# Performance work log

Hardware: AMD Instinct MI355X
Metric: run time of the kernel (lower is better)

Reference implementation:

```python
import jax, jax.numpy as jnp
import numpy as np

N_NODES = 100000
N_EDGES = 1600000
N_FEAT = 16
HEADS = 4


def _feast_conv(x, src, dst, U, c, W, b):
    """FeaStConv: q = softmax_h(u^T(x_j - x_i) + c); out_i = mean_j sum_h q_h * (W_h x_j) + b."""
    n = x.shape[0]
    e = src.shape[0]
    xj = x[src]                                   # [E, Fin] gather
    q = jax.nn.softmax(jnp.matmul(xj - x[dst], U) + c, axis=-1)   # [E, H]
    xs = jnp.matmul(xj, W).reshape(e, HEADS, -1)  # [E, H, Fout]
    msg = jnp.einsum('eh,eho->eo', q, xs)         # [E, Fout]
    deg = jax.ops.segment_sum(jnp.ones((e,), x.dtype), dst, num_segments=n)
    agg = jax.ops.segment_sum(msg, dst, num_segments=n)
    return agg / jnp.maximum(deg, 1.0)[:, None] + b


def setup_inputs() -> dict:
    key = jax.random.key(0)
    ks = jax.random.split(key, 32)
    s = 0.1
    d = {
        'x': jax.random.normal(ks[0], (N_NODES, N_FEAT), jnp.float32),
        'edge_index': jax.random.randint(ks[1], (2, N_EDGES), 0, N_NODES, jnp.int32),
        # conv1: 16 -> 16
        'U1': jax.random.normal(ks[2], (N_FEAT, HEADS), jnp.float32) * s,
        'c1': jnp.zeros((HEADS,), jnp.float32),
        'W1': jax.random.normal(ks[3], (N_FEAT, HEADS * 16), jnp.float32) * s,
        'b1': jnp.zeros((16,), jnp.float32),
        # conv2: 16 -> 32
        'U2': jax.random.normal(ks[4], (16, HEADS), jnp.float32) * s,
        'c2': jnp.zeros((HEADS,), jnp.float32),
        'W2': jax.random.normal(ks[5], (16, HEADS * 32), jnp.float32) * s,
        'b2': jnp.zeros((32,), jnp.float32),
        # conv3: 32 -> 64
        'U3': jax.random.normal(ks[6], (32, HEADS), jnp.float32) * s,
        'c3': jnp.zeros((HEADS,), jnp.float32),
        'W3': jax.random.normal(ks[7], (32, HEADS * 64), jnp.float32) * s,
        'b3': jnp.zeros((64,), jnp.float32),
        # linear tail 64->32->16->8->4->1
        'lw1': jax.random.normal(ks[8], (64, 32), jnp.float32) * s,
        'lb1': jnp.zeros((32,), jnp.float32),
        'lw2': jax.random.normal(ks[9], (32, 16), jnp.float32) * s,
        'lb2': jnp.zeros((16,), jnp.float32),
        'lw3': jax.random.normal(ks[10], (16, 8), jnp.float32) * s,
        'lb3': jnp.zeros((8,), jnp.float32),
        'lw4': jax.random.normal(ks[11], (8, 4), jnp.float32) * s,
        'lb4': jnp.zeros((4,), jnp.float32),
        'lw5': jax.random.normal(ks[12], (4, 1), jnp.float32) * s,
        'lb5': jnp.zeros((1,), jnp.float32),
    }
    return d


def reference(x, edge_index, U1, c1, W1, b1, U2, c2, W2, b2, U3, c3, W3, b3,
              lw1, lb1, lw2, lb2, lw3, lb3, lw4, lb4, lw5, lb5):
    src, dst = edge_index[0], edge_index[1]
    h = jax.nn.relu(_feast_conv(x, src, dst, U1, c1, W1, b1))
    h = jax.nn.relu(_feast_conv(h, src, dst, U2, c2, W2, b2))
    h = jax.nn.relu(_feast_conv(h, src, dst, U3, c3, W3, b3))
    # dropout disabled (inference / drop_bool=False): Linear+ReLU tail
    h = jax.nn.relu(jnp.matmul(h, lw1) + lb1)
    h = jax.nn.relu(jnp.matmul(h, lw2) + lb2)
    h = jax.nn.relu(jnp.matmul(h, lw3) + lb3)
    h = jax.nn.relu(jnp.matmul(h, lw4) + lb4)
    return jax.nn.sigmoid(jnp.matmul(h, lw5) + lb5)   # [N, 1]
```

## Files before the change

### kernel.cpp

```cpp
#include <hip/hip_runtime.h>
#include <math.h>

#define N_NODES 100000
#define N_EDGES 1600000
#define HEADS 4
#define NBKT ((N_NODES + 255) / 256)
#define CHUNK_E 4096
#define NCHUNK ((N_EDGES + CHUNK_E - 1) / CHUNK_E)
#define GN ((N_NODES + 255) / 256)

typedef unsigned short ushort_t;
typedef unsigned char  uchar_t;

__device__ __forceinline__ ushort_t f2bf(float x) {
    unsigned u = __float_as_uint(x);
    u += 0x7FFF + ((u >> 16) & 1);
    return (ushort_t)(u >> 16);
}
__device__ __forceinline__ float bf2f(ushort_t v) {
    return __uint_as_float(((unsigned)v) << 16);
}
__device__ __forceinline__ void unpack2(unsigned u, float& lo, float& hi) {
    lo = __uint_as_float(u << 16);
    hi = __uint_as_float(u & 0xffff0000u);
}
__device__ __forceinline__ uchar_t f2fp8(float x) {
    if (x <= 0.0f) return 0;
    unsigned u = __float_as_uint(x) + (1u << 19);
    int e = (int)(u >> 23) - 127 + 15;
    if (e <= 0) return 0;
    if (e > 31) return (uchar_t)255;
    return (uchar_t)((e << 3) | ((u >> 20) & 7));
}
__device__ __forceinline__ float fp8d(uchar_t b) {
    unsigned v = (((unsigned)(b >> 3) + 112u) << 23) | ((unsigned)(b & 7) << 20);
    return (b == 0) ? 0.0f : __uint_as_float(v);
}


__global__ __launch_bounds__(256) void bhist_pcast_kernel(
        const int* __restrict__ dst, int* __restrict__ hist_rows,
        const float* __restrict__ x, const float* __restrict__ U,
        float* __restrict__ p, ushort_t* __restrict__ xbf)
{
    __shared__ int h[NBKT];
    if (blockIdx.x < NCHUNK) {
        for (int i = threadIdx.x; i < NBKT; i += 256) h[i] = 0;
        __syncthreads();
        int base = blockIdx.x * CHUNK_E;
        #pragma unroll
        for (int j = 0; j < CHUNK_E / 256; j++) {
            int e = base + j * 256 + threadIdx.x;
            if (e < N_EDGES) atomicAdd(&h[dst[e] >> 8], 1);
        }
        __syncthreads();
        for (int i = threadIdx.x; i < NBKT; i += 256)
            hist_rows[(size_t)blockIdx.x * NBKT + i] = h[i];
    } else {
        int n = (blockIdx.x - NCHUNK) * 256 + threadIdx.x;
        if (n >= N_NODES) return;
        float a0 = 0, a1 = 0, a2 = 0, a3 = 0;
        const float* hr = x + (size_t)n * 16;
        float xv[16];
        #pragma unroll
        for (int f = 0; f < 16; f++) {
            xv[f] = hr[f];
            a0 += xv[f] * U[f * 4 + 0];
            a1 += xv[f] * U[f * 4 + 1];
            a2 += xv[f] * U[f * 4 + 2];
            a3 += xv[f] * U[f * 4 + 3];
        }
        *(float4*)(p + (size_t)n * 4) = make_float4(a0, a1, a2, a3);
        #pragma unroll
        for (int j = 0; j < 4; j++) {
            ushort4 u;
            u.x = f2bf(xv[4 * j + 0]); u.y = f2bf(xv[4 * j + 1]);
            u.z = f2bf(xv[4 * j + 2]); u.w = f2bf(xv[4 * j + 3]);
            *(ushort4*)(xbf + (size_t)n * 16 + 4 * j) = u;
        }
    }
}


__global__ __launch_bounds__(512) void bscan_kernel(const int* __restrict__ hist_rows,
                                                    int* __restrict__ bucket_base,
                                                    int* __restrict__ bucket_cursor) {
    __shared__ int tmp[512];
    int i = threadIdx.x;
    int v = 0;
    if (i < NBKT)
        for (int r = 0; r < NCHUNK; r++) v += hist_rows[(size_t)r * NBKT + i];
    tmp[i] = v;
    __syncthreads();
    for (int off = 1; off < 512; off <<= 1) {
        int t = (i >= off) ? tmp[i - off] : 0;
        __syncthreads();
        tmp[i] += t;
        __syncthreads();
    }
    int excl = tmp[i] - v;
    if (i < NBKT) { bucket_base[i] = excl; bucket_cursor[i] = excl; }
    if (i == NBKT) bucket_base[NBKT] = N_EDGES;
}


__global__ __launch_bounds__(256) void partition_kernel(const int* __restrict__ src,
                                                        const int* __restrict__ dst,
                                                        int* __restrict__ bucket_cursor,
                                                        int* __restrict__ csr_tmp) {
    constexpr int EPT = CHUNK_E / 256;
    __shared__ int h[NBKT];
    __shared__ int gbase[NBKT];
    __shared__ int rcnt[NBKT];
    for (int i = threadIdx.x; i < NBKT; i += 256) { h[i] = 0; rcnt[i] = 0; }
    __syncthreads();
    int base = blockIdx.x * CHUNK_E;
    int d[EPT], s[EPT];
    #pragma unroll
    for (int j = 0; j < EPT; j++) {
        int e = base + j * 256 + threadIdx.x;
        d[j] = (e < N_EDGES) ? dst[e] : -1;
        s[j] = (e < N_EDGES) ? src[e] : 0;
        if (d[j] >= 0) atomicAdd(&h[d[j] >> 8], 1);
    }
    __syncthreads();
    for (int i = threadIdx.x; i < NBKT; i += 256)
        if (h[i]) gbase[i] = atomicAdd(&bucket_cursor[i], h[i]);
    __syncthreads();
    #pragma unroll
    for (int j = 0; j < EPT; j++) {
        if (d[j] >= 0) {
            int b = d[j] >> 8;
            int r = atomicAdd(&rcnt[b], 1);
            csr_tmp[gbase[b] + r] = ((d[j] & 255) << 20) | s[j];
        }
    }
}


__global__ __launch_bounds__(256) void bucket_build_kernel(const int* __restrict__ bucket_base,
                                                           const int* __restrict__ csr_tmp,
                                                           int* __restrict__ rowptr,
                                                           int* __restrict__ csr_src) {
    __shared__ int cnt[256];
    __shared__ int tscan[256];
    __shared__ int exc[256];
    __shared__ int stage[8192];
    int b = blockIdx.x;
    int rbeg = bucket_base[b], rend = bucket_base[b + 1];
    int sz = rend - rbeg;
    int tid = threadIdx.x;

    cnt[tid] = 0;
    __syncthreads();
    for (int k = rbeg + tid; k < rend; k += 256) atomicAdd(&cnt[csr_tmp[k] >> 20], 1);
    __syncthreads();
    int v = cnt[tid];
    tscan[tid] = v;
    __syncthreads();
    for (int off = 1; off < 256; off <<= 1) {
        int t = (tid >= off) ? tscan[tid - off] : 0;
        __syncthreads();
        tscan[tid] += t;
        __syncthreads();
    }
    int ex = tscan[tid] - v;
    int node = b * 256 + tid;
    if (node < N_NODES) rowptr[node] = rbeg + ex;
    if (b == 0 && tid == 0) rowptr[N_NODES] = N_EDGES;
    exc[tid] = ex;
    cnt[tid] = 0;
    __syncthreads();

    if (sz <= 8192) {
        for (int k = rbeg + tid; k < rend; k += 256) {
            int pk = csr_tmp[k];
            int dl = pk >> 20;
            int r  = atomicAdd(&cnt[dl], 1);
            stage[exc[dl] + r] = pk & ((1 << 20) - 1);
        }
        __syncthreads();
        for (int i = tid; i < sz; i += 256) csr_src[rbeg + i] = stage[i];
    } else {
        for (int k = rbeg + tid; k < rend; k += 256) {
            int pk = csr_tmp[k];
            int dl = pk >> 20;
            int r  = atomicAdd(&cnt[dl], 1);
            csr_src[rbeg + exc[dl] + r] = pk & ((1 << 20) - 1);
        }
    }
}


template<int FIN, int FMT>
__global__ __launch_bounds__(256) void zgather_kernel(
        const int* __restrict__ rowptr, const int* __restrict__ csr_src,
        const float* __restrict__ p, const float* __restrict__ cvec,
        const void* __restrict__ hraw,
        ushort_t* __restrict__ z)
{
    constexpr int NPB   = 256 / FIN;
    constexpr int CHUNK = 512;
    __shared__ int    sbeg[NPB + 1];
    __shared__ float4 qs[CHUNK];
    __shared__ int    ssrc[CHUNK];

    const ushort_t* hbf = (const ushort_t*)hraw;
    const uchar_t*  hf8 = (const uchar_t*)hraw;

    int tid  = threadIdx.x;
    int nloc = tid / FIN;
    int f    = tid - nloc * FIN;
    int n0   = blockIdx.x * NPB;
    int n    = n0 + nloc;

    if (tid <= NPB) {
        int idx = n0 + tid;
        sbeg[tid] = rowptr[idx > N_NODES ? N_NODES : idx];
    }
    float c0 = cvec[0], c1 = cvec[1], c2 = cvec[2], c3 = cvec[3];
    __syncthreads();

    int BB = sbeg[0], BE = sbeg[NPB];
    int beg = sbeg[nloc], end = sbeg[nloc + 1];
    float a0 = 0, a1 = 0, a2 = 0, a3 = 0;

    for (int cbase = BB; cbase < BE; cbase += CHUNK) {
        int cend = min(cbase + CHUNK, BE);
        __syncthreads();
        for (int k = cbase + tid; k < cend; k += 256) {
            int s = csr_src[k];
            int lo = 0, hi = NPB;
            while (hi - lo > 1) { int mid = (lo + hi) >> 1; if (k < sbeg[mid]) hi = mid; else lo = mid; }
            float4 ps = *(const float4*)(p + (size_t)s * 4);
            float4 pd = *(const float4*)(p + (size_t)(n0 + lo) * 4);
            float l0 = ps.x - pd.x + c0;
            float l1 = ps.y - pd.y + c1;
            float l2 = ps.z - pd.z + c2;
            float l3 = ps.w - pd.w + c3;
            float m  = fmaxf(fmaxf(l0, l1), fmaxf(l2, l3));
            float e0 = __expf(l0 - m), e1 = __expf(l1 - m);
            float e2 = __expf(l2 - m), e3 = __expf(l3 - m);
            float deg = (float)(sbeg[lo + 1] - sbeg[lo]);
            float inv = 1.0f / (fmaxf(deg, 1.0f) * (e0 + e1 + e2 + e3));
            qs[k - cbase]   = make_float4(e0 * inv, e1 * inv, e2 * inv, e3 * inv);
            ssrc[k - cbase] = s;
        }
        __syncthreads();
        int kb = (beg > cbase ? beg : cbase) - cbase;
        int ke = (end < cend ? end : cend) - cbase;
        int k = kb;
        for (; k + 8 <= ke; k += 8) {
            float xv8[8];
            if (FMT == 0) {
                ushort_t u[8];
                #pragma unroll
                for (int j = 0; j < 8; j++) u[j] = hbf[(size_t)ssrc[k + j] * FIN + f];
                #pragma unroll
                for (int j = 0; j < 8; j++) xv8[j] = bf2f(u[j]);
            } else {
                uchar_t u[8];
                #pragma unroll
                for (int j = 0; j < 8; j++) u[j] = hf8[(size_t)ssrc[k + j] * FIN + f];
                #pragma unroll
                for (int j = 0; j < 8; j++) xv8[j] = fp8d(u[j]);
            }
            #pragma unroll
            for (int j = 0; j < 8; j++) {
                float4 q = qs[k + j];
                a0 += q.x * xv8[j]; a1 += q.y * xv8[j];
                a2 += q.z * xv8[j]; a3 += q.w * xv8[j];
            }
        }
        for (; k < ke; k++) {
            float xv = (FMT == 0) ? bf2f(hbf[(size_t)ssrc[k] * FIN + f])
                                  : fp8d(hf8[(size_t)ssrc[k] * FIN + f]);
            float4 q = qs[k];
            a0 += q.x * xv; a1 += q.y * xv; a2 += q.z * xv; a3 += q.w * xv;
        }
    }

    if (n < N_NODES) {
        size_t base = (size_t)n * (4 * FIN) + f;
        z[base]           = f2bf(a0);
        z[base + FIN]     = f2bf(a1);
        z[base + 2 * FIN] = f2bf(a2);
        z[base + 3 * FIN] = f2bf(a3);
    }
}


template<int FIN, int FOUT, int MODE>
__global__ __launch_bounds__(256, 4) void post_kernel(
        const ushort_t* __restrict__ z,
        const float* __restrict__ W,
        const float* __restrict__ b,
        ushort_t* __restrict__ out_bf,
        uchar_t* __restrict__ out_f8,
        const float* __restrict__ Unext,
        float* __restrict__ pnext)
{
    constexpr int K   = 4 * FIN;
    constexpr int OL  = FOUT / 4;
    constexpr int NPB = 4 * (256 / OL);
    constexpr int WSZ = FIN * 4 * FOUT;
    constexpr bool PNEXT = (MODE != 0);
    __shared__ float Wp[WSZ];
    __shared__ float htile[PNEXT ? NPB * FOUT : 1];
    __shared__ float Uloc[PNEXT ? FOUT * 4 : 1];
    for (int i = threadIdx.x; i < WSZ; i += 256) {
        int f = i / (4 * FOUT);
        int r = i - f * (4 * FOUT);
        int h = r / FOUT;
        int o = r - h * FOUT;
        Wp[(h * FIN + f) * FOUT + o] = W[i];
    }
    if (PNEXT) {
        for (int i = threadIdx.x; i < FOUT * 4; i += 256) Uloc[i] = Unext[i];
    }
    __syncthreads();

    int ol = threadIdx.x % OL;
    int g  = threadIdx.x / OL;
    int n0 = blockIdx.x * NPB + g * 4;

    float4 bv = *(const float4*)(b + 4 * ol);
    float4 acc[4];
    const ushort_t* zr[4];
    #pragma unroll
    for (int j = 0; j < 4; j++) {
        acc[j] = make_float4(0.f, 0.f, 0.f, 0.f);
        int nn = n0 + j; if (nn > N_NODES - 1) nn = N_NODES - 1;
        zr[j] = z + (size_t)nn * K;
    }

    #pragma unroll 2
    for (int kq = 0; kq < K / 4; kq++) {
        float zv[4][4];
        #pragma unroll
        for (int j = 0; j < 4; j++) {
            ushort4 zu = *(const ushort4*)(zr[j] + 4 * kq);
            zv[j][0] = bf2f(zu.x); zv[j][1] = bf2f(zu.y);
            zv[j][2] = bf2f(zu.z); zv[j][3] = bf2f(zu.w);
        }
        #pragma unroll
        for (int jj = 0; jj < 4; jj++) {
            float4 wv = *(const float4*)(Wp + (4 * kq + jj) * FOUT + 4 * ol);
            #pragma unroll
            for (int j = 0; j < 4; j++) {
                float s = zv[j][jj];
                acc[j].x += s * wv.x;
                acc[j].y += s * wv.y;
                acc[j].z += s * wv.z;
                acc[j].w += s * wv.w;
            }
        }
    }

    #pragma unroll
    for (int j = 0; j < 4; j++) {
        int nn = n0 + j;
        float4 r;
        r.x = fmaxf(acc[j].x + bv.x, 0.0f);
        r.y = fmaxf(acc[j].y + bv.y, 0.0f);
        r.z = fmaxf(acc[j].z + bv.z, 0.0f);
        r.w = fmaxf(acc[j].w + bv.w, 0.0f);
        if (PNEXT)
            *(float4*)(htile + (g * 4 + j) * FOUT + 4 * ol) = r;
        if (nn < N_NODES) {
            if (MODE == 2) {
                uchar_t u0 = f2fp8(r.x), u1 = f2fp8(r.y), u2 = f2fp8(r.z), u3 = f2fp8(r.w);
                unsigned pk = (unsigned)u0 | ((unsigned)u1 << 8) |
                              ((unsigned)u2 << 16) | ((unsigned)u3 << 24);
                *(unsigned*)(out_f8 + (size_t)nn * FOUT + 4 * ol) = pk;
            } else {
                ushort4 u;
                u.x = f2bf(r.x); u.y = f2bf(r.y); u.z = f2bf(r.z); u.w = f2bf(r.w);
                *(ushort4*)(out_bf + (size_t)nn * FOUT + 4 * ol) = u;
            }
        }
    }

    if (PNEXT) {
        __syncthreads();
        int tid = threadIdx.x;
        if (tid < NPB) {
            int nn = blockIdx.x * NPB + tid;
            if (nn < N_NODES) {
                float a0 = 0, a1 = 0, a2 = 0, a3 = 0;
                const float* hr = htile + tid * FOUT;
                #pragma unroll
                for (int f = 0; f < FOUT; f++) {
                    float xv = hr[f];
                    a0 += xv * Uloc[f * 4 + 0];
                    a1 += xv * Uloc[f * 4 + 1];
                    a2 += xv * Uloc[f * 4 + 2];
                    a3 += xv * Uloc[f * 4 + 3];
                }
                *(float4*)(pnext + (size_t)nn * 4) = make_float4(a0, a1, a2, a3);
            }
        }
    }
}


__global__ __launch_bounds__(256) void tail_kernel(
        const ushort_t* __restrict__ h,
        const float* __restrict__ lw1, const float* __restrict__ lb1,
        const float* __restrict__ lw2, const float* __restrict__ lb2,
        const float* __restrict__ lw3, const float* __restrict__ lb3,
        const float* __restrict__ lw4, const float* __restrict__ lb4,
        const float* __restrict__ lw5, const float* __restrict__ lb5,
        float* __restrict__ out)
{
    __shared__ float w1[64 * 32], w2[32 * 16], w3[16 * 8], w4[8 * 4], w5[4];
    __shared__ float B1[32], B2[16], B3[8], B4[4], B5[1];
    for (int i = threadIdx.x; i < 64 * 32; i += blockDim.x) w1[i] = lw1[i];
    for (int i = threadIdx.x; i < 32 * 16; i += blockDim.x) w2[i] = lw2[i];
    for (int i = threadIdx.x; i < 16 * 8;  i += blockDim.x) w3[i] = lw3[i];
    for (int i = threadIdx.x; i < 8 * 4;   i += blockDim.x) w4[i] = lw4[i];
    for (int i = threadIdx.x; i < 4;       i += blockDim.x) w5[i] = lw5[i];
    for (int i = threadIdx.x; i < 32; i += blockDim.x) B1[i] = lb1[i];
    for (int i = threadIdx.x; i < 16; i += blockDim.x) B2[i] = lb2[i];
    for (int i = threadIdx.x; i < 8;  i += blockDim.x) B3[i] = lb3[i];
    for (int i = threadIdx.x; i < 4;  i += blockDim.x) B4[i] = lb4[i];
    if (threadIdx.x == 0) B5[0] = lb5[0];
    __syncthreads();

    int n = blockIdx.x * blockDim.x + threadIdx.x;
    if (n >= N_NODES) return;

    float a[64];
    const uint4* hrow = (const uint4*)(h + (size_t)n * 64);
    #pragma unroll
    for (int j = 0; j < 8; j++) {
        uint4 v = hrow[j];
        unpack2(v.x, a[8 * j + 0], a[8 * j + 1]);
        unpack2(v.y, a[8 * j + 2], a[8 * j + 3]);
        unpack2(v.z, a[8 * j + 4], a[8 * j + 5]);
        unpack2(v.w, a[8 * j + 6], a[8 * j + 7]);
    }

    float t1[32];
    for (int o = 0; o < 32; o++) {
        float acc = B1[o];
        #pragma unroll
        for (int i = 0; i < 64; i++) acc += a[i] * w1[i * 32 + o];
        t1[o] = fmaxf(acc, 0.0f);
    }
    float t2[16];
    for (int o = 0; o < 16; o++) {
        float acc = B2[o];
        #pragma unroll
        for (int i = 0; i < 32; i++) acc += t1[i] * w2[i * 16 + o];
        t2[o] = fmaxf(acc, 0.0f);
    }
    float t3[8];
    for (int o = 0; o < 8; o++) {
        float acc = B3[o];
        #pragma unroll
        for (int i = 0; i < 16; i++) acc += t2[i] * w3[i * 8 + o];
        t3[o] = fmaxf(acc, 0.0f);
    }
    float t4[4];
    for (int o = 0; o < 4; o++) {
        float acc = B4[o];
        #pragma unroll
        for (int i = 0; i < 8; i++) acc += t3[i] * w4[i * 4 + o];
        t4[o] = fmaxf(acc, 0.0f);
    }
    float zf = B5[0];
    #pragma unroll
    for (int i = 0; i < 4; i++) zf += t4[i] * w5[i];
    out[n] = 1.0f / (1.0f + expf(-zf));
}


extern "C" void kernel_launch(void* const* d_in, const int* in_sizes, int n_in,
                              void* d_out, int out_size, void* d_ws, size_t ws_size,
                              hipStream_t stream) {
    const float* x   = (const float*)d_in[0];
    const int*   ei  = (const int*)d_in[1];
    const int*   src = ei;
    const int*   dst = ei + N_EDGES;
    const float* U1 = (const float*)d_in[2];  const float* c1 = (const float*)d_in[3];
    const float* W1 = (const float*)d_in[4];  const float* b1 = (const float*)d_in[5];
    const float* U2 = (const float*)d_in[6];  const float* c2 = (const float*)d_in[7];
    const float* W2 = (const float*)d_in[8];  const float* b2 = (const float*)d_in[9];
    const float* U3 = (const float*)d_in[10]; const float* c3 = (const float*)d_in[11];
    const float* W3 = (const float*)d_in[12]; const float* b3 = (const float*)d_in[13];
    const float* lw1 = (const float*)d_in[14]; const float* lb1 = (const float*)d_in[15];
    const float* lw2 = (const float*)d_in[16]; const float* lb2 = (const float*)d_in[17];
    const float* lw3 = (const float*)d_in[18]; const float* lb3 = (const float*)d_in[19];
    const float* lw4 = (const float*)d_in[20]; const float* lb4 = (const float*)d_in[21];
    const float* lw5 = (const float*)d_in[22]; const float* lb5 = (const float*)d_in[23];

    char* ws = (char*)d_ws;
    size_t off = 0;
    auto alloc = [&](size_t bytes) -> void* {
        void* ptr = (void*)(ws + off);
        off += (bytes + 255) & ~(size_t)255;
        return ptr;
    };
    int*      hist_rows     = (int*)alloc((size_t)NCHUNK * NBKT * 4);
    int*      bucket_base   = (int*)alloc((size_t)(NBKT + 1) * 4);
    int*      bucket_cursor = (int*)alloc((size_t)NBKT * 4);
    int*      csr_tmp       = (int*)alloc((size_t)N_EDGES * 4);
    int*      rowptr        = (int*)alloc(((size_t)N_NODES + 1) * 4);
    int*      csr_src       = (int*)alloc((size_t)N_EDGES * 4);
    float*    p             = (float*)alloc((size_t)N_NODES * 4 * 4);
    ushort_t* z             = (ushort_t*)alloc((size_t)N_NODES * 128 * 2);
    ushort_t* xbf           = (ushort_t*)alloc((size_t)N_NODES * 16 * 2);
    ushort_t* h1bf          = (ushort_t*)alloc((size_t)N_NODES * 16 * 2);
    uchar_t*  h2f8          = (uchar_t*)alloc((size_t)N_NODES * 32);
    ushort_t* h3bf          = (ushort_t*)alloc((size_t)N_NODES * 64 * 2);
    (void)ws_size;

    const int B = 256;

    bhist_pcast_kernel<<<NCHUNK + GN, B, 0, stream>>>(dst, hist_rows, x, U1, p, xbf);
    bscan_kernel<<<1, 512, 0, stream>>>(hist_rows, bucket_base, bucket_cursor);
    partition_kernel<<<NCHUNK, B, 0, stream>>>(src, dst, bucket_cursor, csr_tmp);
    bucket_build_kernel<<<NBKT, B, 0, stream>>>(bucket_base, csr_tmp, rowptr, csr_src);

    const int ZG16 = (N_NODES + (256 / 16) - 1) / (256 / 16);
    const int ZG32 = (N_NODES + (256 / 32) - 1) / (256 / 32);
    const int NPB1 = 4 * (256 / (16 / 4));
    const int NPB2 = 4 * (256 / (32 / 4));
    const int NPB3 = 4 * (256 / (64 / 4));

    zgather_kernel<16, 0><<<ZG16, B, 0, stream>>>(rowptr, csr_src, p, c1, xbf, z);
    post_kernel<16, 16, 1><<<(N_NODES + NPB1 - 1) / NPB1, B, 0, stream>>>(
        z, W1, b1, h1bf, nullptr, U2, p);

    zgather_kernel<16, 0><<<ZG16, B, 0, stream>>>(rowptr, csr_src, p, c2, h1bf, z);
    post_kernel<16, 32, 2><<<(N_NODES + NPB2 - 1) / NPB2, B, 0, stream>>>(
        z, W2, b2, nullptr, h2f8, U3, p);

    zgather_kernel<32, 1><<<ZG32, B, 0, stream>>>(rowptr, csr_src, p, c3, h2f8, z);
    post_kernel<32, 64, 0><<<(N_NODES + NPB3 - 1) / NPB3, B, 0, stream>>>(
        z, W3, b3, h3bf, nullptr, nullptr, nullptr);

    tail_kernel<<<GN, B, 0, stream>>>(h3bf, lw1, lb1, lw2, lb2, lw3, lb3,
                                      lw4, lb4, lw5, lb5, (float*)d_out);
}
```

Before: 350.7 us.

## Give each gather thread four contiguous features with vector loads

Each thread in the z-gather kernel now handles four contiguous features of a node instead of one. Features are fetched with 8-byte (bf16) or 4-byte (fp8) vector loads, results are written with ushort4 stores, and the per-edge softmax weights are reused across four features per thread. Blocks now cover four times as many nodes and the shared-memory edge chunk is doubled to 1024. In exchange each thread holds 16 accumulators, which raises register pressure, and per-node edge loops are serialized over fewer lanes, so degree imbalance weighs more.

```diff
diff --git a/kernel.cpp b/kernel.cpp
--- a/kernel.cpp
+++ b/kernel.cpp
@@ -199,8 +199,9 @@
         const void* __restrict__ hraw,
         ushort_t* __restrict__ z)
 {
-    constexpr int NPB   = 256 / FIN;
-    constexpr int CHUNK = 512;
+    constexpr int LPN   = FIN / 4;
+    constexpr int NPB   = 256 / LPN;
+    constexpr int CHUNK = 1024;
     __shared__ int    sbeg[NPB + 1];
     __shared__ float4 qs[CHUNK];
     __shared__ int    ssrc[CHUNK];
@@ -209,21 +210,22 @@
     const uchar_t*  hf8 = (const uchar_t*)hraw;
 
     int tid  = threadIdx.x;
-    int nloc = tid / FIN;
-    int f    = tid - nloc * FIN;
+    int nloc = tid / LPN;
+    int fl   = (tid - nloc * LPN) * 4;
     int n0   = blockIdx.x * NPB;
     int n    = n0 + nloc;
 
-    if (tid <= NPB) {
-        int idx = n0 + tid;
-        sbeg[tid] = rowptr[idx > N_NODES ? N_NODES : idx];
+    for (int i = tid; i <= NPB; i += 256) {
+        int idx = n0 + i;
+        sbeg[i] = rowptr[idx > N_NODES ? N_NODES : idx];
     }
     float c0 = cvec[0], c1 = cvec[1], c2 = cvec[2], c3 = cvec[3];
     __syncthreads();
 
     int BB = sbeg[0], BE = sbeg[NPB];
     int beg = sbeg[nloc], end = sbeg[nloc + 1];
-    float a0 = 0, a1 = 0, a2 = 0, a3 = 0;
+
+    float4 acc0 = make_float4(0, 0, 0, 0), acc1 = acc0, acc2 = acc0, acc3 = acc0;
 
     for (int cbase = BB; cbase < BE; cbase += CHUNK) {
         int cend = min(cbase + CHUNK, BE);
@@ -250,42 +252,76 @@
         int kb = (beg > cbase ? beg : cbase) - cbase;
         int ke = (end < cend ? end : cend) - cbase;
         int k = kb;
-        for (; k + 8 <= ke; k += 8) {
-            float xv8[8];
+        for (; k + 4 <= ke; k += 4) {
+            float xv[4][4];
             if (FMT == 0) {
-                ushort_t u[8];
+                uint2 r[4];
                 #pragma unroll
-                for (int j = 0; j < 8; j++) u[j] = hbf[(size_t)ssrc[k + j] * FIN + f];
+                for (int j = 0; j < 4; j++)
+                    r[j] = *(const uint2*)(hbf + (size_t)ssrc[k + j] * FIN + fl);
                 #pragma unroll
-                for (int j = 0; j < 8; j++) xv8[j] = bf2f(u[j]);
+                for (int j = 0; j < 4; j++) {
+                    unpack2(r[j].x, xv[j][0], xv[j][1]);
+                    unpack2(r[j].y, xv[j][2], xv[j][3]);
+                }
             } else {
-                uchar_t u[8];
+                unsigned r[4];
                 #pragma unroll
-                for (int j = 0; j < 8; j++) u[j] = hf8[(size_t)ssrc[k + j] * FIN + f];
+                for (int j = 0; j < 4; j++)
+                    r[j] = *(const unsigned*)(hf8 + (size_t)ssrc[k + j] * FIN + fl);
                 #pragma unroll
-                for (int j = 0; j < 8; j++) xv8[j] = fp8d(u[j]);
+                for (int j = 0; j < 4; j++) {
+                    xv[j][0] = fp8d((uchar_t)(r[j] & 255));
+                    xv[j][1] = fp8d((uchar_t)((r[j] >> 8) & 255));
+                    xv[j][2] = fp8d((uchar_t)((r[j] >> 16) & 255));
+                    xv[j][3] = fp8d((uchar_t)(r[j] >> 24));
+                }
             }
             #pragma unroll
-            for (int j = 0; j < 8; j++) {
+            for (int j = 0; j < 4; j++) {
                 float4 q = qs[k + j];
-                a0 += q.x * xv8[j]; a1 += q.y * xv8[j];
-                a2 += q.z * xv8[j]; a3 += q.w * xv8[j];
+                acc0.x += q.x * xv[j][0]; acc0.y += q.x * xv[j][1];
+                acc0.z += q.x * xv[j][2]; acc0.w += q.x * xv[j][3];
+                acc1.x += q.y * xv[j][0]; acc1.y += q.y * xv[j][1];
+                acc1.z += q.y * xv[j][2]; acc1.w += q.y * xv[j][3];
+                acc2.x += q.z * xv[j][0]; acc2.y += q.z * xv[j][1];
+                acc2.z += q.z * xv[j][2]; acc2.w += q.z * xv[j][3];
+                acc3.x += q.w * xv[j][0]; acc3.y += q.w * xv[j][1];
+                acc3.z += q.w * xv[j][2]; acc3.w += q.w * xv[j][3];
             }
         }
         for (; k < ke; k++) {
-            float xv = (FMT == 0) ? bf2f(hbf[(size_t)ssrc[k] * FIN + f])
-                                  : fp8d(hf8[(size_t)ssrc[k] * FIN + f]);
+            float x0, x1, x2, x3;
+            if (FMT == 0) {
+                uint2 r = *(const uint2*)(hbf + (size_t)ssrc[k] * FIN + fl);
+                unpack2(r.x, x0, x1);
+                unpack2(r.y, x2, x3);
+            } else {
+                unsigned r = *(const unsigned*)(hf8 + (size_t)ssrc[k] * FIN + fl);
+                x0 = fp8d((uchar_t)(r & 255));
+                x1 = fp8d((uchar_t)((r >> 8) & 255));
+                x2 = fp8d((uchar_t)((r >> 16) & 255));
+                x3 = fp8d((uchar_t)(r >> 24));
+            }
             float4 q = qs[k];
-            a0 += q.x * xv; a1 += q.y * xv; a2 += q.z * xv; a3 += q.w * xv;
+            acc0.x += q.x * x0; acc0.y += q.x * x1; acc0.z += q.x * x2; acc0.w += q.x * x3;
+            acc1.x += q.y * x0; acc1.y += q.y * x1; acc1.z += q.y * x2; acc1.w += q.y * x3;
+            acc2.x += q.z * x0; acc2.y += q.z * x1; acc2.z += q.z * x2; acc2.w += q.z * x3;
+            acc3.x += q.w * x0; acc3.y += q.w * x1; acc3.z += q.w * x2; acc3.w += q.w * x3;
         }
     }
 
     if (n < N_NODES) {
-        size_t base = (size_t)n * (4 * FIN) + f;
-        z[base]           = f2bf(a0);
-        z[base + FIN]     = f2bf(a1);
-        z[base + 2 * FIN] = f2bf(a2);
-        z[base + 3 * FIN] = f2bf(a3);
+        size_t base = (size_t)n * (4 * FIN) + fl;
+        ushort4 u;
+        u.x = f2bf(acc0.x); u.y = f2bf(acc0.y); u.z = f2bf(acc0.z); u.w = f2bf(acc0.w);
+        *(ushort4*)(z + base) = u;
+        u.x = f2bf(acc1.x); u.y = f2bf(acc1.y); u.z = f2bf(acc1.z); u.w = f2bf(acc1.w);
+        *(ushort4*)(z + base + FIN) = u;
+        u.x = f2bf(acc2.x); u.y = f2bf(acc2.y); u.z = f2bf(acc2.z); u.w = f2bf(acc2.w);
+        *(ushort4*)(z + base + 2 * FIN) = u;
+        u.x = f2bf(acc3.x); u.y = f2bf(acc3.y); u.z = f2bf(acc3.z); u.w = f2bf(acc3.w);
+        *(ushort4*)(z + base + 3 * FIN) = u;
     }
 }
 
@@ -523,8 +559,8 @@
     partition_kernel<<<NCHUNK, B, 0, stream>>>(src, dst, bucket_cursor, csr_tmp);
     bucket_build_kernel<<<NBKT, B, 0, stream>>>(bucket_base, csr_tmp, rowptr, csr_src);
 
-    const int ZG16 = (N_NODES + (256 / 16) - 1) / (256 / 16);
-    const int ZG32 = (N_NODES + (256 / 32) - 1) / (256 / 32);
+    const int ZG16 = (N_NODES + 63) / 64;
+    const int ZG32 = (N_NODES + 31) / 32;
     const int NPB1 = 4 * (256 / (16 / 4));
     const int NPB2 = 4 * (256 / (32 / 4));
     const int NPB3 = 4 * (256 / (64 / 4));
```

New measurement: 337.5 us. -3.7%, faster.
